# Kernel optimization log

Hardware: AMD Instinct MI355X
Metric: run time of the kernel (lower is better)

Reference implementation:

```python
import jax, jax.numpy as jnp
import numpy as np

EPS_NORM = 1e-12  # torch F.normalize eps
EPS_BN = 1e-5     # torch BatchNorm eps


def _normalize(x, axis=-1):
    n = jnp.linalg.norm(x, axis=axis, keepdims=True)
    return x / jnp.maximum(n, EPS_NORM)


def _bn(x, axes):
    # training-mode BatchNorm with gamma=1, beta=0 (bn_weight_init=1)
    m = jnp.mean(x, axis=axes, keepdims=True)
    v = jnp.var(x, axis=axes, keepdims=True)
    return (x - m) * jax.lax.rsqrt(v + EPS_BN)


def _gather(points, idx):
    # points (B,N,C), idx (B,M,K) -> (B,M,K,C)
    B = points.shape[0]
    return points[jnp.arange(B)[:, None, None], idx]


def _vi_transform(localized_xyz, gathered_norm, sparse_xyz_norm):
    # localized_xyz, gathered_norm: (B,M,K,3); sparse_xyz_norm: (B,M,3)
    r_hat = _normalize(localized_xyz, axis=3)
    n_s = sparse_xyz_norm[:, :, None, :]                      # (B,M,1,3)
    proj = jnp.sum(n_s * r_hat, axis=3, keepdims=True)        # (B,M,K,1)
    v_miu = _normalize(n_s - proj * r_hat, axis=3)
    w_miu = _normalize(jnp.cross(r_hat, v_miu), axis=3)
    t1 = jnp.sum(gathered_norm * n_s, axis=3, keepdims=True)
    t2 = jnp.sum(r_hat * n_s, axis=3, keepdims=True)
    t3 = jnp.sum(r_hat * gathered_norm, axis=3, keepdims=True)
    t4 = jnp.sum(localized_xyz * n_s, axis=3, keepdims=True)
    t5 = jnp.sum(gathered_norm * r_hat, axis=3, keepdims=True)
    t6 = jnp.sum(gathered_norm * v_miu, axis=3, keepdims=True)
    t7 = jnp.sum(gathered_norm * w_miu, axis=3, keepdims=True)
    t8 = jnp.sum(localized_xyz * jnp.cross(gathered_norm, jnp.broadcast_to(n_s, gathered_norm.shape)), axis=3, keepdims=True)
    t9 = jnp.linalg.norm(localized_xyz, axis=3, keepdims=True)
    return jnp.concatenate([t1, t2, t3, t4, t5, t6, t7, t8, t9, localized_xyz], axis=3)  # (B,M,K,12)


def setup_inputs():
    key = jax.random.key(0)
    ks = jax.random.split(key, 12)
    B, N, K = 2, 40000, 16
    Cin, Cmlp, Cw, Cout = 64, 64, 16, 128
    s = 0.05
    return {
        'dense_xyz': jax.random.normal(ks[0], (B, N, 3), jnp.float32),
        'dense_feats': jax.random.normal(ks[1], (B, N, Cin), jnp.float32),
        'dense_xyz_norm': _normalize(jax.random.normal(ks[2], (B, N, 3), jnp.float32)),
        'nei_inds': jax.random.randint(ks[3], (B, N, K), 0, N),
        'w_pe': jax.random.normal(ks[4], (Cin + 12, Cmlp), jnp.float32) * s,
        'b_pe': jnp.zeros((Cmlp,), jnp.float32),
        'w1': jax.random.normal(ks[5], (12, 8), jnp.float32) * s,
        'b1': jnp.zeros((8,), jnp.float32),
        'w2': jax.random.normal(ks[6], (8, 8), jnp.float32) * s,
        'b2': jnp.zeros((8,), jnp.float32),
        'w3': jax.random.normal(ks[7], (8, Cw), jnp.float32) * s,
        'b3': jnp.zeros((Cw,), jnp.float32),
        'w_lin': jax.random.normal(ks[8], (Cmlp * Cw, Cout), jnp.float32) * s,
        'b_lin': jnp.zeros((Cout,), jnp.float32),
    }


def reference(dense_xyz, dense_feats, dense_xyz_norm, nei_inds,
              w_pe, b_pe, w1, b1, w2, b2, w3, b3, w_lin, b_lin):
    B, N, _ = dense_xyz.shape
    # gather neighbors (sparse_xyz=None path -> M = N)
    gathered_xyz = _gather(dense_xyz, nei_inds)                 # (B,N,K,3)
    localized_xyz = gathered_xyz - dense_xyz[:, :, None, :]
    gathered_norm = _gather(dense_xyz_norm, nei_inds)
    weightNetInput = _vi_transform(localized_xyz, gathered_norm, dense_xyz_norm)  # (B,N,K,12)

    # USE_PE: concat feats with VI features, one Linear_BN + relu
    gathered_feat = _gather(dense_feats, nei_inds)              # (B,N,K,Cin)
    gathered_feat = jnp.concatenate([gathered_feat, weightNetInput], axis=-1)
    gathered_feat = jax.nn.relu(_bn(gathered_feat @ w_pe + b_pe, (0, 1, 2)))  # (B,N,K,64)

    # WeightNet: 12 -> 8 -> 8 -> 16, each Linear_BN + relu
    w = weightNetInput
    for W, b in ((w1, b1), (w2, b2), (w3, b3)):
        w = jax.nn.relu(_bn(w @ W + b, (0, 1, 2)))              # (B,N,K,16)

    # weighted aggregation over K, then final Linear_BN(1d) + relu
    new_feat = jnp.einsum('bnkc,bnkw->bncw', gathered_feat, w).reshape(B, N, -1)  # (B,N,1024)
    new_feat = jax.nn.relu(_bn(new_feat @ w_lin + b_lin, (0, 1)))                 # (B,N,128)
    return new_feat, weightNetInput
```

## Files before the change

### kernel.cpp

```cpp
#include <hip/hip_runtime.h>
#include <hip/hip_bf16.h>

#define NPK   1280000
#define NPTS  80000
#define NK    640000
#define NPN   40000


typedef __attribute__((ext_vector_type(8))) short bf16x8;
typedef __attribute__((ext_vector_type(4))) float f32x4;

__device__ inline unsigned short f2bf(float f){
  union { float f; unsigned u; } v; v.f = f;
  unsigned r = v.u + 0x7FFFu + ((v.u >> 16) & 1u);
  return (unsigned short)(r >> 16);
}
__device__ inline float bf2f(unsigned short u){
  union { unsigned u; float f; } v; v.u = ((unsigned)u) << 16; return v.f;
}

__device__ inline float wred(float v){
  #pragma unroll
  for (int m = 32; m; m >>= 1) v += __shfl_xor(v, m, 64);
  return v;
}

__global__ __launch_bounds__(256) void kP(const float* __restrict__ xyz,
                                          const float* __restrict__ nrm,
                                          float* __restrict__ P){
  int r = blockIdx.x*256 + threadIdx.x;
  if (r >= NPTS) return;
  float4 a = make_float4(xyz[r*3], xyz[r*3+1], xyz[r*3+2], 0.f);
  float4 b = make_float4(nrm[r*3], nrm[r*3+1], nrm[r*3+2], 0.f);
  ((float4*)P)[r*2]   = a;
  ((float4*)P)[r*2+1] = b;
}

__global__ __launch_bounds__(256) void kWT(const float* __restrict__ wl,
                                           unsigned short* __restrict__ wlT){
  int idx = blockIdx.x*256 + threadIdx.x;
  float v = wl[idx];
  int k = idx >> 7, n = idx & 127;
  wlT[(size_t)n*1024 + k] = f2bf(v);
}

__global__ __launch_bounds__(256, 2) void kF(const float* __restrict__ feats,
                                             const float* __restrict__ w_pe,
                                             const float* __restrict__ b_pe,
                                             float* __restrict__ F){
  __shared__ float af[4][64];
  int tid = threadIdx.x, w = tid >> 6, lane = tid & 63;
  float wf[64];
  #pragma unroll
  for (int i = 0; i < 64; ++i) wf[i] = w_pe[i*64 + lane];
  float bp = b_pe[lane];
  int wid = blockIdx.x*4 + w;
  for (int r = wid; r < NPTS; r += 2560){
    af[w][lane] = feats[(size_t)r*64 + lane];
    const float4* ar = (const float4*)&af[w][0];
    float acc = bp;
    #pragma unroll
    for (int i = 0; i < 16; ++i){
      float4 a4 = ar[i];
      acc = fmaf(a4.x, wf[4*i+0], acc);
      acc = fmaf(a4.y, wf[4*i+1], acc);
      acc = fmaf(a4.z, wf[4*i+2], acc);
      acc = fmaf(a4.w, wf[4*i+3], acc);
    }
    F[(size_t)r*64 + lane] = acc;
  }
}

__global__ __launch_bounds__(256) void k_vi(const float* __restrict__ P,
                                            const int*   __restrict__ nei,
                                            const float* __restrict__ w1,
                                            const float* __restrict__ b1,
                                            float* __restrict__ out2,
                                            float* __restrict__ stats){
  int tid = threadIdx.x;
  float s[8] = {0,0,0,0,0,0,0,0}, q[8] = {0,0,0,0,0,0,0,0};
  #pragma unroll 1
  for (int it = 0; it < 8; ++it){
    int g = blockIdx.x*256 + tid + it*160000;
    int b  = g / NK;
    int nk = g - b*NK;
    int n  = nk >> 4;
    int pr = b*NPN + n;
    int jr = b*NPN + nei[g];
    float4 c0 = ((const float4*)P)[pr*2], c1 = ((const float4*)P)[pr*2+1];
    float4 j0 = ((const float4*)P)[jr*2], j1 = ((const float4*)P)[jr*2+1];
    float nx = c1.x, ny = c1.y, nz = c1.z;
    float lx = j0.x - c0.x, ly = j0.y - c0.y, lz = j0.z - c0.z;
    float gx = j1.x, gy = j1.y, gz = j1.z;
    float t9 = sqrtf(lx*lx + ly*ly + lz*lz);
    float ir = 1.0f / fmaxf(t9, 1e-12f);
    float rx = lx*ir, ry = ly*ir, rz = lz*ir;
    float t2 = nx*rx + ny*ry + nz*rz;
    float vx = nx - t2*rx, vy = ny - t2*ry, vz = nz - t2*rz;
    float vn = sqrtf(vx*vx + vy*vy + vz*vz);
    float iv = 1.0f / fmaxf(vn, 1e-12f);
    vx *= iv; vy *= iv; vz *= iv;
    float wx = ry*vz - rz*vy, wy = rz*vx - rx*vz, wz = rx*vy - ry*vx;
    float wn = sqrtf(wx*wx + wy*wy + wz*wz);
    float iw = 1.0f / fmaxf(wn, 1e-12f);
    wx *= iw; wy *= iw; wz *= iw;
    float t1 = gx*nx + gy*ny + gz*nz;
    float t3 = rx*gx + ry*gy + rz*gz;
    float t4 = lx*nx + ly*ny + lz*nz;
    float t6 = gx*vx + gy*vy + gz*vz;
    float t7 = gx*wx + gy*wy + gz*wz;
    float ccx = gy*nz - gz*ny, ccy = gz*nx - gx*nz, ccz = gx*ny - gy*nx;
    float t8 = lx*ccx + ly*ccy + lz*ccz;
    float wni[12] = {t1,t2,t3,t4,t3,t6,t7,t8,t9,lx,ly,lz};
    float4* o = (float4*)(out2 + (size_t)g*12);
    o[0] = make_float4(t1,t2,t3,t4);
    o[1] = make_float4(t3,t6,t7,t8);
    o[2] = make_float4(t9,lx,ly,lz);
    #pragma unroll
    for (int jj = 0; jj < 8; ++jj){
      float a = b1[jj];
      #pragma unroll
      for (int i = 0; i < 12; ++i) a = fmaf(wni[i], w1[i*8 + jj], a);
      s[jj] += a; q[jj] += a*a;
    }
  }
  __shared__ float red[4][16];
  int lane = tid & 63, wv = tid >> 6;
  float st[16];
  #pragma unroll
  for (int i = 0; i < 8; ++i){ st[i] = s[i]; st[8+i] = q[i]; }
  #pragma unroll
  for (int i = 0; i < 16; ++i) st[i] = wred(st[i]);
  if (lane == 0){
    #pragma unroll
    for (int i = 0; i < 16; ++i) red[wv][i] = st[i];
  }
  __syncthreads();
  if (tid < 16)
    atomicAdd(&stats[128 + tid], red[0][tid] + red[1][tid] + red[2][tid] + red[3][tid]);
}

__global__ __launch_bounds__(256) void k_pe2(const float* __restrict__ F,
                                             const int*   __restrict__ nei,
                                             const float* __restrict__ out2,
                                             const float* __restrict__ w_pe,
                                             float* __restrict__ stats){
  int tid = threadIdx.x, lane = tid & 63;
  float gw[12];
  #pragma unroll
  for (int i = 0; i < 12; ++i) gw[i] = w_pe[(64+i)*64 + lane];
  float s = 0.f, q = 0.f;
  int wid = blockIdx.x*4 + (tid >> 6);
  #pragma unroll 4
  for (int pk = wid; pk < NPK; pk += 8192){
    int row = (pk >= NK ? NPN : 0) + nei[pk];
    float xv = F[(size_t)row*64 + lane];
    const float4* wp = (const float4*)(out2 + (size_t)pk*12);
    float4 u0 = wp[0], u1 = wp[1], u2 = wp[2];
    float g = u0.x*gw[0];
    g = fmaf(u0.y, gw[1],  g); g = fmaf(u0.z, gw[2],  g); g = fmaf(u0.w, gw[3],  g);
    g = fmaf(u1.x, gw[4],  g); g = fmaf(u1.y, gw[5],  g); g = fmaf(u1.z, gw[6],  g);
    g = fmaf(u1.w, gw[7],  g); g = fmaf(u2.x, gw[8],  g); g = fmaf(u2.y, gw[9],  g);
    g = fmaf(u2.z, gw[10], g); g = fmaf(u2.w, gw[11], g);
    float x = xv + g;
    s += x; q += x*x;
  }
  __shared__ float r[256];
  r[tid] = s; __syncthreads();
  if (tid < 64) atomicAdd(&stats[tid],      r[tid] + r[tid+64] + r[tid+128] + r[tid+192]);
  __syncthreads();
  r[tid] = q; __syncthreads();
  if (tid < 64) atomicAdd(&stats[64 + tid], r[tid] + r[tid+64] + r[tid+128] + r[tid+192]);
}

__global__ __launch_bounds__(256) void k3a(const float* __restrict__ out2,
                                           const float* __restrict__ w1, const float* __restrict__ b1,
                                           const float* __restrict__ w2, const float* __restrict__ b2,
                                           float* __restrict__ stats){
  int tid = threadIdx.x;
  const float invc = 1.0f/1280000.0f;
  float sc1[8], sh1[8];
  #pragma unroll
  for (int j = 0; j < 8; ++j){
    float m = stats[128+j]*invc, v = stats[136+j]*invc - m*m;
    float c = rsqrtf(fmaxf(v, 0.f) + 1e-5f); sc1[j] = c; sh1[j] = -m*c;
  }
  float s[8] = {0,0,0,0,0,0,0,0}, q[8] = {0,0,0,0,0,0,0,0};
  #pragma unroll 1
  for (int it = 0; it < 8; ++it){
    int g = blockIdx.x*256 + tid + it*160000;
    const float4* wp = (const float4*)(out2 + (size_t)g*12);
    float4 a0 = wp[0], a1 = wp[1], a2 = wp[2];
    float wni[12] = {a0.x,a0.y,a0.z,a0.w,a1.x,a1.y,a1.z,a1.w,a2.x,a2.y,a2.z,a2.w};
    float h1[8];
    #pragma unroll
    for (int j = 0; j < 8; ++j){
      float a = b1[j];
      #pragma unroll
      for (int i = 0; i < 12; ++i) a = fmaf(wni[i], w1[i*8+j], a);
      h1[j] = fmaxf(fmaf(a, sc1[j], sh1[j]), 0.f);
    }
    #pragma unroll
    for (int j = 0; j < 8; ++j){
      float a = b2[j];
      #pragma unroll
      for (int i = 0; i < 8; ++i) a = fmaf(h1[i], w2[i*8+j], a);
      s[j] += a; q[j] += a*a;
    }
  }
  __shared__ float red[4][16];
  int lane = tid & 63, wv = tid >> 6;
  float st[16];
  #pragma unroll
  for (int i = 0; i < 8; ++i){ st[i] = s[i]; st[8+i] = q[i]; }
  #pragma unroll
  for (int i = 0; i < 16; ++i) st[i] = wred(st[i]);
  if (lane == 0){
    #pragma unroll
    for (int i = 0; i < 16; ++i) red[wv][i] = st[i];
  }
  __syncthreads();
  if (tid < 16)
    atomicAdd(&stats[144 + tid], red[0][tid] + red[1][tid] + red[2][tid] + red[3][tid]);
}

__global__ __launch_bounds__(256) void k3b(const float* __restrict__ out2,
                                           const float* __restrict__ w1, const float* __restrict__ b1,
                                           const float* __restrict__ w2, const float* __restrict__ b2,
                                           const float* __restrict__ w3, const float* __restrict__ b3,
                                           float* __restrict__ stats){
  int tid = threadIdx.x;
  const float invc = 1.0f/1280000.0f;
  float sc1[8], sh1[8], sc2[8], sh2[8];
  #pragma unroll
  for (int j = 0; j < 8; ++j){
    float m = stats[128+j]*invc, v = stats[136+j]*invc - m*m;
    float c = rsqrtf(fmaxf(v, 0.f) + 1e-5f); sc1[j] = c; sh1[j] = -m*c;
    m = stats[144+j]*invc; v = stats[152+j]*invc - m*m;
    c = rsqrtf(fmaxf(v, 0.f) + 1e-5f); sc2[j] = c; sh2[j] = -m*c;
  }
  float s[16], q[16];
  #pragma unroll
  for (int j = 0; j < 16; ++j){ s[j] = 0.f; q[j] = 0.f; }
  #pragma unroll 1
  for (int it = 0; it < 8; ++it){
    int g = blockIdx.x*256 + tid + it*160000;
    const float4* wp = (const float4*)(out2 + (size_t)g*12);
    float4 a0 = wp[0], a1 = wp[1], a2 = wp[2];
    float wni[12] = {a0.x,a0.y,a0.z,a0.w,a1.x,a1.y,a1.z,a1.w,a2.x,a2.y,a2.z,a2.w};
    float h1[8], h2[8];
    #pragma unroll
    for (int j = 0; j < 8; ++j){
      float a = b1[j];
      #pragma unroll
      for (int i = 0; i < 12; ++i) a = fmaf(wni[i], w1[i*8+j], a);
      h1[j] = fmaxf(fmaf(a, sc1[j], sh1[j]), 0.f);
    }
    #pragma unroll
    for (int j = 0; j < 8; ++j){
      float a = b2[j];
      #pragma unroll
      for (int i = 0; i < 8; ++i) a = fmaf(h1[i], w2[i*8+j], a);
      h2[j] = fmaxf(fmaf(a, sc2[j], sh2[j]), 0.f);
    }
    #pragma unroll
    for (int j = 0; j < 16; ++j){
      float a = b3[j];
      #pragma unroll
      for (int i = 0; i < 8; ++i) a = fmaf(h2[i], w3[i*16+j], a);
      s[j] += a; q[j] += a*a;
    }
  }
  __shared__ float red[4][32];
  int lane = tid & 63, wv = tid >> 6;
  float st[32];
  #pragma unroll
  for (int i = 0; i < 16; ++i){ st[i] = s[i]; st[16+i] = q[i]; }
  #pragma unroll
  for (int i = 0; i < 32; ++i) st[i] = wred(st[i]);
  if (lane == 0){
    #pragma unroll
    for (int i = 0; i < 32; ++i) red[wv][i] = st[i];
  }
  __syncthreads();
  if (tid < 32)
    atomicAdd(&stats[160 + tid], red[0][tid] + red[1][tid] + red[2][tid] + red[3][tid]);
}

__global__ __launch_bounds__(256) void k3c(const float* __restrict__ out2,
                                           const float* __restrict__ w1, const float* __restrict__ b1,
                                           const float* __restrict__ w2, const float* __restrict__ b2,
                                           const float* __restrict__ w3, const float* __restrict__ b3,
                                           const float* __restrict__ stats,
                                           unsigned short* __restrict__ WGb){
  int idx = blockIdx.x*256 + threadIdx.x;
  const float invc = 1.0f/1280000.0f;
  float sc1[8], sh1[8], sc2[8], sh2[8], sc3[16], sh3[16];
  #pragma unroll
  for (int j = 0; j < 8; ++j){
    float m = stats[128+j]*invc, v = stats[136+j]*invc - m*m;
    float c = rsqrtf(fmaxf(v, 0.f) + 1e-5f); sc1[j] = c; sh1[j] = -m*c;
    m = stats[144+j]*invc; v = stats[152+j]*invc - m*m;
    c = rsqrtf(fmaxf(v, 0.f) + 1e-5f); sc2[j] = c; sh2[j] = -m*c;
  }
  #pragma unroll
  for (int j = 0; j < 16; ++j){
    float m = stats[160+j]*invc, v = stats[176+j]*invc - m*m;
    float c = rsqrtf(fmaxf(v, 0.f) + 1e-5f); sc3[j] = c; sh3[j] = -m*c;
  }
  const float4* wp = (const float4*)(out2 + (size_t)idx*12);
  float4 a0 = wp[0], a1 = wp[1], a2 = wp[2];
  float wni[12] = {a0.x,a0.y,a0.z,a0.w,a1.x,a1.y,a1.z,a1.w,a2.x,a2.y,a2.z,a2.w};
  float h1[8], h2[8], h3[16];
  #pragma unroll
  for (int j = 0; j < 8; ++j){
    float a = b1[j];
    #pragma unroll
    for (int i = 0; i < 12; ++i) a = fmaf(wni[i], w1[i*8+j], a);
    h1[j] = fmaxf(fmaf(a, sc1[j], sh1[j]), 0.f);
  }
  #pragma unroll
  for (int j = 0; j < 8; ++j){
    float a = b2[j];
    #pragma unroll
    for (int i = 0; i < 8; ++i) a = fmaf(h1[i], w2[i*8+j], a);
    h2[j] = fmaxf(fmaf(a, sc2[j], sh2[j]), 0.f);
  }
  #pragma unroll
  for (int j = 0; j < 16; ++j){
    float a = b3[j];
    #pragma unroll
    for (int i = 0; i < 8; ++i) a = fmaf(h2[i], w3[i*16+j], a);
    h3[j] = fmaxf(fmaf(a, sc3[j], sh3[j]), 0.f);
  }
  unsigned pk2[8];
  #pragma unroll
  for (int i = 0; i < 8; ++i)
    pk2[i] = (unsigned)f2bf(h3[2*i]) | ((unsigned)f2bf(h3[2*i+1]) << 16);
  uint4* o = (uint4*)(WGb + (size_t)idx*16);
  o[0] = make_uint4(pk2[0], pk2[1], pk2[2], pk2[3]);
  o[1] = make_uint4(pk2[4], pk2[5], pk2[6], pk2[7]);
}

__global__ __launch_bounds__(256, 2) void k4f(const float* __restrict__ F,
                                              const int*   __restrict__ nei,
                                              const float* __restrict__ out2,
                                              const float* __restrict__ w_pe,
                                              const unsigned short* __restrict__ WGb,
                                              const float* __restrict__ stats,
                                              const unsigned short* __restrict__ wlT,
                                              const float* __restrict__ blin,
                                              float* __restrict__ LP){
  __shared__ short  As[32][1024];
  __shared__ short  Bs[128][32];
  __shared__ float4 wt[4][64];
  __shared__ float  wn[4][192];
  int tid = threadIdx.x, w = tid >> 6, lane = tid & 63;
  char* asb = (char*)&As[0][0];
  char* bsb = (char*)&Bs[0][0];
  const float invc = 1.0f/1280000.0f;
  float sm = stats[lane]*invc, sq = stats[64+lane]*invc;
  float sc = rsqrtf(fmaxf(sq - sm*sm, 0.f) + 1e-5f);
  float sh = -sm*sc;
  float gw[12];
  #pragma unroll
  for (int i = 0; i < 12; ++i) gw[i] = w_pe[(64+i)*64 + lane];
  int p_base = blockIdx.x*32;

  #pragma unroll 1
  for (int pi = 0; pi < 8; ++pi){
    int row = w*8 + pi;
    int p = p_base + row;
    int base = (p >= NPN) ? NPN : 0;
    int nv = nei[p*16 + (lane & 15)];
    float xf[16];
    #pragma unroll
    for (int k = 0; k < 16; ++k){
      int r = base + __shfl(nv, k, 64);
      xf[k] = F[(size_t)r*64 + lane];
    }
    const float* o2 = out2 + (size_t)p*192;
    wn[w][lane]     = o2[lane];
    wn[w][64+lane]  = o2[64+lane];
    wn[w][128+lane] = o2[128+lane];
    ushort4 wv = *(const ushort4*)(WGb + (size_t)p*256 + lane*4);
    wt[w][lane] = make_float4(bf2f(wv.x), bf2f(wv.y), bf2f(wv.z), bf2f(wv.w));
    float m[16];
    #pragma unroll
    for (int i = 0; i < 16; ++i) m[i] = 0.f;
    #pragma unroll 4
    for (int k = 0; k < 16; ++k){
      const float4* u = (const float4*)&wn[w][k*12];
      float4 u0 = u[0], u1 = u[1], u2 = u[2];
      float g = u0.x*gw[0];
      g = fmaf(u0.y, gw[1],  g); g = fmaf(u0.z, gw[2],  g); g = fmaf(u0.w, gw[3],  g);
      g = fmaf(u1.x, gw[4],  g); g = fmaf(u1.y, gw[5],  g); g = fmaf(u1.z, gw[6],  g);
      g = fmaf(u1.w, gw[7],  g); g = fmaf(u2.x, gw[8],  g); g = fmaf(u2.y, gw[9],  g);
      g = fmaf(u2.z, gw[10], g); g = fmaf(u2.w, gw[11], g);
      float pe = fmaxf(fmaf(xf[k] + g, sc, sh), 0.f);
      float4 w0 = wt[w][k*4+0], w1v = wt[w][k*4+1], w2v = wt[w][k*4+2], w3v = wt[w][k*4+3];
      m[0]  = fmaf(pe, w0.x,  m[0]);  m[1]  = fmaf(pe, w0.y,  m[1]);
      m[2]  = fmaf(pe, w0.z,  m[2]);  m[3]  = fmaf(pe, w0.w,  m[3]);
      m[4]  = fmaf(pe, w1v.x, m[4]);  m[5]  = fmaf(pe, w1v.y, m[5]);
      m[6]  = fmaf(pe, w1v.z, m[6]);  m[7]  = fmaf(pe, w1v.w, m[7]);
      m[8]  = fmaf(pe, w2v.x, m[8]);  m[9]  = fmaf(pe, w2v.y, m[9]);
      m[10] = fmaf(pe, w2v.z, m[10]); m[11] = fmaf(pe, w2v.w, m[11]);
      m[12] = fmaf(pe, w3v.x, m[12]); m[13] = fmaf(pe, w3v.y, m[13]);
      m[14] = fmaf(pe, w3v.z, m[14]); m[15] = fmaf(pe, w3v.w, m[15]);
    }
    bf16x8 lo, hi;
    #pragma unroll
    for (int i = 0; i < 8; ++i){ lo[i] = (short)f2bf(m[i]); hi[i] = (short)f2bf(m[8+i]); }
    unsigned xr = (unsigned)((row & 7) << 4);
    unsigned b0 = (unsigned)(row*2048 + lane*32);
    *(bf16x8*)(asb + ( b0        ^ xr)) = lo;
    *(bf16x8*)(asb + ((b0 + 16)  ^ xr)) = hi;
  }
  __syncthreads();

  f32x4 acc[2][2];
  #pragma unroll
  for (int i = 0; i < 2; ++i)
    #pragma unroll
    for (int j = 0; j < 2; ++j) acc[i][j] = (f32x4){0.f,0.f,0.f,0.f};
  int r15 = lane & 15, q = lane >> 4;
  unsigned xrA = (unsigned)((r15 & 7) << 4);
  #pragma unroll 1
  for (int ks = 0; ks < 32; ++ks){
    {
      int n = tid >> 1, kh = tid & 1;
      const unsigned short* src = wlT + (size_t)n*1024 + ks*32 + kh*16;
      bf16x8 v0 = *(const bf16x8*)(src);
      bf16x8 v1 = *(const bf16x8*)(src + 8);
      unsigned bb = (unsigned)(n*64 + kh*32);
      unsigned xb = (unsigned)((n & 3) << 4);
      *(bf16x8*)(bsb + ( bb        ^ xb)) = v0;
      *(bf16x8*)(bsb + ((bb + 16)  ^ xb)) = v1;
    }
    __syncthreads();
    unsigned ka = (unsigned)(ks*64 + q*16);
    bf16x8 a0 = *(const bf16x8*)(asb + ((unsigned)( r15     *2048 + ka) ^ xrA));
    bf16x8 a1 = *(const bf16x8*)(asb + ((unsigned)((16+r15)*2048 + ka) ^ xrA));
    int n0 = w*32 + r15, n1 = n0 + 16;
    bf16x8 b0 = *(const bf16x8*)(bsb + ((unsigned)(n0*64 + q*16) ^ (unsigned)((n0 & 3) << 4)));
    bf16x8 b1 = *(const bf16x8*)(bsb + ((unsigned)(n1*64 + q*16) ^ (unsigned)((n1 & 3) << 4)));
    acc[0][0] = __builtin_amdgcn_mfma_f32_16x16x32_bf16(a0, b0, acc[0][0], 0, 0, 0);
    acc[0][1] = __builtin_amdgcn_mfma_f32_16x16x32_bf16(a0, b1, acc[0][1], 0, 0, 0);
    acc[1][0] = __builtin_amdgcn_mfma_f32_16x16x32_bf16(a1, b0, acc[1][0], 0, 0, 0);
    acc[1][1] = __builtin_amdgcn_mfma_f32_16x16x32_bf16(a1, b1, acc[1][1], 0, 0, 0);
    __syncthreads();
  }
  float bc0 = blin[w*32 + r15], bc1 = blin[w*32 + 16 + r15];
  #pragma unroll
  for (int mi = 0; mi < 2; ++mi){
    #pragma unroll
    for (int j = 0; j < 4; ++j){
      int prow = p_base + mi*16 + q*4 + j;
      LP[(size_t)prow*128 + w*32 + r15]      = acc[mi][0][j] + bc0;
      LP[(size_t)prow*128 + w*32 + 16 + r15] = acc[mi][1][j] + bc1;
    }
  }
}

__global__ __launch_bounds__(256) void k4c(const float* __restrict__ LP,
                                           float* __restrict__ stats){
  int tid = threadIdx.x; int ch = tid & 127; int half = tid >> 7;
  float s = 0.f, q = 0.f;
  for (int p = blockIdx.x*2 + half; p < NPTS; p += gridDim.x*2){
    float v = LP[(size_t)p*128 + ch]; s += v; q += v*v;
  }
  __shared__ float r[256];
  r[tid] = s; __syncthreads();
  if (tid < 128) atomicAdd(&stats[192 + tid], r[tid] + r[tid+128]);
  __syncthreads();
  r[tid] = q; __syncthreads();
  if (tid < 128) atomicAdd(&stats[320 + tid], r[tid] + r[tid+128]);
}

__global__ __launch_bounds__(256) void k5(float* __restrict__ LP,
                                          const float* __restrict__ stats){
  __shared__ float sc[128], sh[128];
  int tid = threadIdx.x;
  if (tid < 128){
    const float invc = 1.0f/80000.0f;
    float s = stats[192+tid]*invc, q = stats[320+tid]*invc;
    float c = rsqrtf(fmaxf(q - s*s, 0.f) + 1e-5f);
    sc[tid] = c; sh[tid] = -s*c;
  }
  __syncthreads();
  for (int g4 = blockIdx.x*256 + tid; g4 < 2560000; g4 += gridDim.x*256){
    int cb = (g4 & 31) * 4;
    float4 v = ((const float4*)LP)[g4];
    float4 o;
    o.x = fmaxf(fmaf(v.x, sc[cb+0], sh[cb+0]), 0.f);
    o.y = fmaxf(fmaf(v.y, sc[cb+1], sh[cb+1]), 0.f);
    o.z = fmaxf(fmaf(v.z, sc[cb+2], sh[cb+2]), 0.f);
    o.w = fmaxf(fmaf(v.w, sc[cb+3], sh[cb+3]), 0.f);
    ((float4*)LP)[g4] = o;
  }
}

extern "C" void kernel_launch(void* const* d_in, const int* in_sizes, int n_in,
                              void* d_out, int out_size, void* d_ws, size_t ws_size,
                              hipStream_t stream){
  const float* xyz   = (const float*)d_in[0];
  const float* feats = (const float*)d_in[1];
  const float* nrm   = (const float*)d_in[2];
  const int*   nei   = (const int*)  d_in[3];
  const float* w_pe  = (const float*)d_in[4];
  const float* b_pe  = (const float*)d_in[5];
  const float* w1    = (const float*)d_in[6];
  const float* b1    = (const float*)d_in[7];
  const float* w2    = (const float*)d_in[8];
  const float* b2    = (const float*)d_in[9];
  const float* w3    = (const float*)d_in[10];
  const float* b3    = (const float*)d_in[11];
  const float* wl    = (const float*)d_in[12];
  const float* blin  = (const float*)d_in[13];

  float* out1 = (float*)d_out;
  float* out2 = out1 + 10240000;

  float* stats        = (float*)d_ws;
  float* F            = stats + 512;
  float* P            = F + (size_t)NPTS*64;
  unsigned short* wlT = (unsigned short*)(P + (size_t)NPTS*8);
  unsigned short* WGb = wlT + 131072;

  hipMemsetAsync(stats, 0, 512*sizeof(float), stream);
  kP   <<<(NPTS+255)/256, 256, 0, stream>>>(xyz, nrm, P);
  kWT  <<<512,  256, 0, stream>>>(wl, wlT);
  kF   <<<640,  256, 0, stream>>>(feats, w_pe, b_pe, F);
  k_vi <<<625,  256, 0, stream>>>(P, nei, w1, b1, out2, stats);
  k_pe2<<<2048, 256, 0, stream>>>(F, nei, out2, w_pe, stats);
  k3a  <<<625,  256, 0, stream>>>(out2, w1, b1, w2, b2, stats);
  k3b  <<<625,  256, 0, stream>>>(out2, w1, b1, w2, b2, w3, b3, stats);
  k3c  <<<5000, 256, 0, stream>>>(out2, w1, b1, w2, b2, w3, b3, stats, WGb);
  k4f  <<<2500, 256, 0, stream>>>(F, nei, out2, w_pe, WGb, stats, wlT, blin, out1);
  k4c  <<<512,  256, 0, stream>>>(out1, stats);
  k5   <<<1280, 256, 0, stream>>>(out1, stats);
}
```

Before: 666.4 us.

## Halve k4f point tile, permute wlT K-order, double k_vi grid

The fused aggregation+GEMM kernel k4f now handles 16 points per block instead of 32. This halves the A-tile in shared memory and raises the launch-bounds occupancy hint to 3 blocks per CU, with twice as many blocks launched. The transposed final weight is stored with a permuted K order so that each lane can write its 16 aggregated channels as two separated 8-element chunks, and the B-tile load uses a new swizzle. k_vi runs twice as many blocks, each doing half the loop iterations. Smaller tiles reuse each loaded B tile less, so global weight traffic per output doubles in exchange for more parallelism.

```diff
diff --git a/kernel.cpp b/kernel.cpp
--- a/kernel.cpp
+++ b/kernel.cpp
@@ -41,7 +41,9 @@
   int idx = blockIdx.x*256 + threadIdx.x;
   float v = wl[idx];
   int k = idx >> 7, n = idx & 127;
-  wlT[(size_t)n*1024 + k] = f2bf(v);
+  int c = k >> 4, w = k & 15;
+  int kp = ((w >> 3) << 9) + (c << 3) + (w & 7);
+  wlT[(size_t)n*1024 + kp] = f2bf(v);
 }
 
 __global__ __launch_bounds__(256, 2) void kF(const float* __restrict__ feats,
@@ -80,8 +82,8 @@
   int tid = threadIdx.x;
   float s[8] = {0,0,0,0,0,0,0,0}, q[8] = {0,0,0,0,0,0,0,0};
   #pragma unroll 1
-  for (int it = 0; it < 8; ++it){
-    int g = blockIdx.x*256 + tid + it*160000;
+  for (int it = 0; it < 4; ++it){
+    int g = blockIdx.x*256 + tid + it*320000;
     int b  = g / NK;
     int nk = g - b*NK;
     int n  = nk >> 4;
@@ -342,7 +344,7 @@
   o[1] = make_uint4(pk2[4], pk2[5], pk2[6], pk2[7]);
 }
 
-__global__ __launch_bounds__(256, 2) void k4f(const float* __restrict__ F,
+__global__ __launch_bounds__(256, 3) void k4f(const float* __restrict__ F,
                                               const int*   __restrict__ nei,
                                               const float* __restrict__ out2,
                                               const float* __restrict__ w_pe,
@@ -351,7 +353,7 @@
                                               const unsigned short* __restrict__ wlT,
                                               const float* __restrict__ blin,
                                               float* __restrict__ LP){
-  __shared__ short  As[32][1024];
+  __shared__ short  As[16][1024];
   __shared__ short  Bs[128][32];
   __shared__ float4 wt[4][64];
   __shared__ float  wn[4][192];
@@ -365,11 +367,11 @@
   float gw[12];
   #pragma unroll
   for (int i = 0; i < 12; ++i) gw[i] = w_pe[(64+i)*64 + lane];
-  int p_base = blockIdx.x*32;
+  int p_base = blockIdx.x*16;
 
   #pragma unroll 1
-  for (int pi = 0; pi < 8; ++pi){
-    int row = w*8 + pi;
+  for (int pi = 0; pi < 4; ++pi){
+    int row = w*4 + pi;
     int p = p_base + row;
     int base = (p >= NPN) ? NPN : 0;
     int nv = nei[p*16 + (lane & 15)];
@@ -412,53 +414,44 @@
     #pragma unroll
     for (int i = 0; i < 8; ++i){ lo[i] = (short)f2bf(m[i]); hi[i] = (short)f2bf(m[8+i]); }
     unsigned xr = (unsigned)((row & 7) << 4);
-    unsigned b0 = (unsigned)(row*2048 + lane*32);
-    *(bf16x8*)(asb + ( b0        ^ xr)) = lo;
-    *(bf16x8*)(asb + ((b0 + 16)  ^ xr)) = hi;
-  }
-  __syncthreads();
-
-  f32x4 acc[2][2];
-  #pragma unroll
-  for (int i = 0; i < 2; ++i)
-    #pragma unroll
-    for (int j = 0; j < 2; ++j) acc[i][j] = (f32x4){0.f,0.f,0.f,0.f};
+    unsigned b0 = (unsigned)(row*2048 + lane*16);
+    *(bf16x8*)(asb + ( b0          ^ xr)) = lo;
+    *(bf16x8*)(asb + ((b0 + 1024)  ^ xr)) = hi;
+  }
+  __syncthreads();
+
+  f32x4 acc0 = (f32x4){0.f,0.f,0.f,0.f}, acc1 = (f32x4){0.f,0.f,0.f,0.f};
   int r15 = lane & 15, q = lane >> 4;
   unsigned xrA = (unsigned)((r15 & 7) << 4);
   #pragma unroll 1
   for (int ks = 0; ks < 32; ++ks){
     {
-      int n = tid >> 1, kh = tid & 1;
-      const unsigned short* src = wlT + (size_t)n*1024 + ks*32 + kh*16;
-      bf16x8 v0 = *(const bf16x8*)(src);
-      bf16x8 v1 = *(const bf16x8*)(src + 8);
-      unsigned bb = (unsigned)(n*64 + kh*32);
-      unsigned xb = (unsigned)((n & 3) << 4);
-      *(bf16x8*)(bsb + ( bb        ^ xb)) = v0;
-      *(bf16x8*)(bsb + ((bb + 16)  ^ xb)) = v1;
+      #pragma unroll
+      for (int e = 0; e < 2; ++e){
+        int idx = tid + e*256;
+        int n = idx >> 2, sub = idx & 3;
+        bf16x8 v = *(const bf16x8*)(wlT + (size_t)n*1024 + ks*32 + sub*8);
+        unsigned virt = (unsigned)(idx*16);
+        *(bf16x8*)(bsb + (virt ^ (((virt >> 7) & 3u) << 4))) = v;
+      }
     }
     __syncthreads();
     unsigned ka = (unsigned)(ks*64 + q*16);
-    bf16x8 a0 = *(const bf16x8*)(asb + ((unsigned)( r15     *2048 + ka) ^ xrA));
-    bf16x8 a1 = *(const bf16x8*)(asb + ((unsigned)((16+r15)*2048 + ka) ^ xrA));
+    bf16x8 a0 = *(const bf16x8*)(asb + ((unsigned)(r15*2048 + ka) ^ xrA));
     int n0 = w*32 + r15, n1 = n0 + 16;
-    bf16x8 b0 = *(const bf16x8*)(bsb + ((unsigned)(n0*64 + q*16) ^ (unsigned)((n0 & 3) << 4)));
-    bf16x8 b1 = *(const bf16x8*)(bsb + ((unsigned)(n1*64 + q*16) ^ (unsigned)((n1 & 3) << 4)));
-    acc[0][0] = __builtin_amdgcn_mfma_f32_16x16x32_bf16(a0, b0, acc[0][0], 0, 0, 0);
-    acc[0][1] = __builtin_amdgcn_mfma_f32_16x16x32_bf16(a0, b1, acc[0][1], 0, 0, 0);
-    acc[1][0] = __builtin_amdgcn_mfma_f32_16x16x32_bf16(a1, b0, acc[1][0], 0, 0, 0);
-    acc[1][1] = __builtin_amdgcn_mfma_f32_16x16x32_bf16(a1, b1, acc[1][1], 0, 0, 0);
+    unsigned v0 = (unsigned)(n0*64 + q*16), v1 = (unsigned)(n1*64 + q*16);
+    bf16x8 b0 = *(const bf16x8*)(bsb + (v0 ^ (((v0 >> 7) & 3u) << 4)));
+    bf16x8 b1 = *(const bf16x8*)(bsb + (v1 ^ (((v1 >> 7) & 3u) << 4)));
+    acc0 = __builtin_amdgcn_mfma_f32_16x16x32_bf16(a0, b0, acc0, 0, 0, 0);
+    acc1 = __builtin_amdgcn_mfma_f32_16x16x32_bf16(a0, b1, acc1, 0, 0, 0);
     __syncthreads();
   }
   float bc0 = blin[w*32 + r15], bc1 = blin[w*32 + 16 + r15];
   #pragma unroll
-  for (int mi = 0; mi < 2; ++mi){
-    #pragma unroll
-    for (int j = 0; j < 4; ++j){
-      int prow = p_base + mi*16 + q*4 + j;
-      LP[(size_t)prow*128 + w*32 + r15]      = acc[mi][0][j] + bc0;
-      LP[(size_t)prow*128 + w*32 + 16 + r15] = acc[mi][1][j] + bc1;
-    }
+  for (int j = 0; j < 4; ++j){
+    int prow = p_base + q*4 + j;
+    LP[(size_t)prow*128 + w*32 + r15]      = acc0[j] + bc0;
+    LP[(size_t)prow*128 + w*32 + 16 + r15] = acc1[j] + bc1;
   }
 }
 
@@ -531,12 +524,12 @@
   kP   <<<(NPTS+255)/256, 256, 0, stream>>>(xyz, nrm, P);
   kWT  <<<512,  256, 0, stream>>>(wl, wlT);
   kF   <<<640,  256, 0, stream>>>(feats, w_pe, b_pe, F);
-  k_vi <<<625,  256, 0, stream>>>(P, nei, w1, b1, out2, stats);
+  k_vi <<<1250, 256, 0, stream>>>(P, nei, w1, b1, out2, stats);
   k_pe2<<<2048, 256, 0, stream>>>(F, nei, out2, w_pe, stats);
   k3a  <<<625,  256, 0, stream>>>(out2, w1, b1, w2, b2, stats);
   k3b  <<<625,  256, 0, stream>>>(out2, w1, b1, w2, b2, w3, b3, stats);
   k3c  <<<5000, 256, 0, stream>>>(out2, w1, b1, w2, b2, w3, b3, stats, WGb);
-  k4f  <<<2500, 256, 0, stream>>>(F, nei, out2, w_pe, WGb, stats, wlT, blin, out1);
+  k4f  <<<5000, 256, 0, stream>>>(F, nei, out2, w_pe, WGb, stats, wlT, blin, out1);
   k4c  <<<512,  256, 0, stream>>>(out1, stats);
   k5   <<<1280, 256, 0, stream>>>(out1, stats);
 }
```

Measured after the change: 684.2 us. +2.7%, slower.
